# Optimization experiments

Hardware: AMD Instinct MI355X
Metric: run time of the kernel (lower is better)

The kernel has to match this reference:

```python
import jax, jax.numpy as jnp
import numpy as np

NEG_SLOPE = 0.2
LN_EPS = 1e-5


def gat_conv(x, src, dst, n_nodes, W, a_src, a_dst, b, concat):
    # W: [F_in, H*C]; a_src, a_dst: [H, C]; b: [H*C] if concat else [C]
    H, C = a_src.shape
    h = (x @ W).reshape(-1, H, C)                      # [N, H, C]
    # per-node attention scores, gathered per edge
    s_src = jnp.einsum('nhc,hc->nh', h, a_src)          # [N, H]
    s_dst = jnp.einsum('nhc,hc->nh', h, a_dst)          # [N, H]
    e = jax.nn.leaky_relu(s_src[src] + s_dst[dst], NEG_SLOPE)  # [E, H]
    # segment softmax over incoming edges of each dst node
    e_max = jax.ops.segment_max(e, dst, num_segments=n_nodes)  # [N, H]
    w = jnp.exp(e - e_max[dst])
    denom = jax.ops.segment_sum(w, dst, num_segments=n_nodes)
    alpha = w / (denom[dst] + 1e-16)                    # [E, H]
    # weighted scatter-aggregate of source messages
    msg = h[src] * alpha[:, :, None]                    # [E, H, C]
    out = jax.ops.segment_sum(msg, dst, num_segments=n_nodes)  # [N, H, C]
    out = out.reshape(n_nodes, H * C) if concat else out.mean(axis=1)
    return out + b


def layer_norm(x, g, b):
    mu = x.mean(-1, keepdims=True)
    var = ((x - mu) ** 2).mean(-1, keepdims=True)
    return (x - mu) * jax.lax.rsqrt(var + LN_EPS) * g + b


def setup_inputs() -> dict:
    key = jax.random.key(0)
    ks = jax.random.split(key, 16)
    N, E, F_in = 50000, 400000, 128
    H1, C1 = 4, 128          # conv1: heads=4, hidden=128, concat -> 512
    C2 = 64                  # conv2: heads=1, out=64
    sd = lambda fan: 1.0 / np.sqrt(fan)
    inp = {
        'x': jax.random.normal(ks[0], (N, F_in), jnp.float32),
        'edge_index': jax.random.randint(ks[1], (2, E), 0, N, jnp.int64),
        'num_nodes': N,
        'W1': jax.random.normal(ks[2], (F_in, H1 * C1), jnp.float32) * sd(F_in),
        'a_src1': jax.random.normal(ks[3], (H1, C1), jnp.float32) * sd(C1),
        'a_dst1': jax.random.normal(ks[4], (H1, C1), jnp.float32) * sd(C1),
        'b1': jnp.zeros((H1 * C1,), jnp.float32),
        'W2': jax.random.normal(ks[5], (H1 * C1, C2), jnp.float32) * sd(H1 * C1),
        'a_src2': jax.random.normal(ks[6], (1, C2), jnp.float32) * sd(C2),
        'a_dst2': jax.random.normal(ks[7], (1, C2), jnp.float32) * sd(C2),
        'b2': jnp.zeros((C2,), jnp.float32),
        'Wm1': jax.random.normal(ks[8], (C2, 32), jnp.float32) * sd(C2),
        'bm1': jnp.zeros((32,), jnp.float32),
        'g_ln': jnp.ones((32,), jnp.float32),
        'b_ln': jnp.zeros((32,), jnp.float32),
        'Wm2': jax.random.normal(ks[9], (32, 16), jnp.float32) * sd(32),
        'bm2': jnp.zeros((16,), jnp.float32),
    }
    return inp


def reference(x, edge_index, num_nodes, W1, a_src1, a_dst1, b1, W2, a_src2, a_dst2, b2, Wm1, bm1, g_ln, b_ln, Wm2, bm2):
    N = num_nodes
    # PyG GATConv add_self_loops=True
    loop = jnp.arange(N, dtype=edge_index.dtype)
    src = jnp.concatenate([edge_index[0], loop])
    dst = jnp.concatenate([edge_index[1], loop])
    # dropout layers are identity in eval mode
    h = jax.nn.elu(gat_conv(x, src, dst, N, W1, a_src1, a_dst1, b1, concat=True))
    h = jax.nn.elu(gat_conv(h, src, dst, N, W2, a_src2, a_dst2, b2, concat=False))
    h = jax.nn.relu(layer_norm(h @ Wm1 + bm1, g_ln, b_ln))
    return h @ Wm2 + bm2  # [N, 2*n_spectral_dims]
```

## Files before the change

### kernel.cpp

```cpp
#include <hip/hip_runtime.h>
#include <cmath>


#define F_IN 128
#define H1   4
#define C1   128
#define D1   512
#define C2   64
#define DM1  32
#define DM2  16

#define LRELU(x) ((x) > 0.f ? (x) : 0.2f * (x))

typedef float f32x4 __attribute__((ext_vector_type(4)));
typedef short short8 __attribute__((ext_vector_type(8)));

static __device__ __forceinline__ float bf2f(unsigned short u) {
    return __builtin_bit_cast(float, (unsigned)u << 16);
}
static __device__ __forceinline__ unsigned short f2bf(float f) {
    unsigned u = __builtin_bit_cast(unsigned, f);
    u = (u + 0x7fffu + ((u >> 16) & 1u)) >> 16;
    return (unsigned short)u;
}
static __device__ __forceinline__ float bflo(unsigned d) {
    return __builtin_bit_cast(float, d << 16);
}
static __device__ __forceinline__ float bfhi(unsigned d) {
    return __builtin_bit_cast(float, d & 0xffff0000u);
}

__global__ void k_detect(const void* ei, int E, int* flag) {
    __shared__ int any;
    if (threadIdx.x == 0) any = 0;
    __syncthreads();
    const int* p = (const int*)ei;
    int cnt = E < 4096 ? E : 4096;
    int stride = E / cnt;
    int local = 0;
    for (int i = threadIdx.x; i < cnt; i += blockDim.x) {
        long long idx = (long long)i * stride;
        local |= p[2 * idx + 1];
    }
    if (local) atomicOr(&any, 1);
    __syncthreads();
    if (threadIdx.x == 0) *flag = (any == 0) ? 1 : 0;
}

__global__ void k_convert_prep(const void* ei, const int* flag, int E, int N,
                               int* src32, int* dst32, int* deg, int* rank32,
                               const float* __restrict__ x,
                               const float* __restrict__ W1,
                               const float* __restrict__ W2,
                               unsigned short* __restrict__ xb,
                               unsigned short* __restrict__ W1t,
                               unsigned short* __restrict__ W2t, int n8) {
    int i = blockIdx.x * blockDim.x + threadIdx.x;
    int Etot = E + N;
    if (i < Etot) {
        int s, d;
        if (i < E) {
            if (*flag) {
                const long long* q = (const long long*)ei;
                s = (int)q[i];
                d = (int)q[(size_t)E + i];
            } else {
                const int* q = (const int*)ei;
                s = q[i];
                d = q[(size_t)E + i];
            }
        } else {
            s = i - E;
            d = i - E;
        }
        src32[i] = s;
        dst32[i] = d;
        rank32[i] = atomicAdd(&deg[d], 1);
        return;
    }
    int i1 = i - Etot;
    if (i1 < n8) {
        const float4* p = (const float4*)(x + (size_t)i1 * 8);
        float4 a = p[0], b = p[1];
        unsigned short r[8] = {f2bf(a.x), f2bf(a.y), f2bf(a.z), f2bf(a.w),
                               f2bf(b.x), f2bf(b.y), f2bf(b.z), f2bf(b.w)};
        *(short8*)(xb + (size_t)i1 * 8) = *(const short8*)r;
        return;
    }
    int i2 = i1 - n8;
    if (i2 < F_IN * D1) {
        int nn = i2 / F_IN, kk = i2 - nn * F_IN;
        W1t[i2] = f2bf(W1[(size_t)kk * D1 + nn]);
        return;
    }
    int i3 = i2 - F_IN * D1;
    if (i3 < D1 * C2) {
        int nn = i3 / D1, kk = i3 - nn * D1;
        W2t[i3] = f2bf(W2[(size_t)kk * C2 + nn]);
    }
}

__global__ __launch_bounds__(256) void k_scan1(const int* __restrict__ deg,
                                               int* __restrict__ bsum, int N) {
    int t = threadIdx.x;
    int base = blockIdx.x * 1024 + t * 4;
    int s = 0;
    if (base + 3 < N) {
        int4 v = *(const int4*)&deg[base];
        s = v.x + v.y + v.z + v.w;
    } else {
        for (int k = 0; k < 4; k++)
            if (base + k < N) s += deg[base + k];
    }
#pragma unroll
    for (int o = 1; o < 64; o <<= 1) s += __shfl_xor(s, o, 64);
    __shared__ int ws[4];
    if ((t & 63) == 0) ws[t >> 6] = s;
    __syncthreads();
    if (t == 0) bsum[blockIdx.x] = ws[0] + ws[1] + ws[2] + ws[3];
}

__global__ __launch_bounds__(1024) void k_scan2(const int* __restrict__ bsum,
                                                int* __restrict__ boff, int nb) {
    __shared__ int wsum[16];
    __shared__ int woff[16];
    int t = threadIdx.x, lane = t & 63, wid = t >> 6;
    int v = (t < nb) ? bsum[t] : 0;
    int x = v;
#pragma unroll
    for (int o = 1; o < 64; o <<= 1) {
        int tv = __shfl_up(x, o, 64);
        if (lane >= o) x += tv;
    }
    if (lane == 63) wsum[wid] = x;
    __syncthreads();
    if (wid == 0) {
        int y = (lane < 16) ? wsum[lane] : 0;
        int z = y;
#pragma unroll
        for (int o = 1; o < 16; o <<= 1) {
            int tv = __shfl_up(z, o, 64);
            if (lane >= o) z += tv;
        }
        if (lane < 16) woff[lane] = z - y;
    }
    __syncthreads();
    if (t < nb) boff[t] = woff[wid] + x - v;
}

__global__ __launch_bounds__(256) void k_scan3(const int* __restrict__ deg,
                                               const int* __restrict__ boff,
                                               int* __restrict__ rowstart, int N,
                                               int Etot) {
    int t = threadIdx.x, lane = t & 63, wid = t >> 6;
    int base = blockIdx.x * 1024 + t * 4;
    int v0 = 0, v1 = 0, v2 = 0, v3 = 0;
    if (base + 3 < N) {
        int4 v = *(const int4*)&deg[base];
        v0 = v.x; v1 = v.y; v2 = v.z; v3 = v.w;
    } else {
        if (base + 0 < N) v0 = deg[base + 0];
        if (base + 1 < N) v1 = deg[base + 1];
        if (base + 2 < N) v2 = deg[base + 2];
        if (base + 3 < N) v3 = deg[base + 3];
    }
    int s4 = v0 + v1 + v2 + v3;
    int x = s4;
#pragma unroll
    for (int o = 1; o < 64; o <<= 1) {
        int tv = __shfl_up(x, o, 64);
        if (lane >= o) x += tv;
    }
    __shared__ int ws[4];
    if (lane == 63) ws[wid] = x;
    __syncthreads();
    int woff = 0;
#pragma unroll
    for (int w = 0; w < 4; w++)
        if (w < wid) woff += ws[w];
    int ex = boff[blockIdx.x] + woff + (x - s4);
    int e0 = ex, e1 = ex + v0, e2 = e1 + v1, e3 = e2 + v2;
    if (base + 0 < N) rowstart[base + 0] = e0;
    if (base + 1 < N) rowstart[base + 1] = e1;
    if (base + 2 < N) rowstart[base + 2] = e2;
    if (base + 3 < N) rowstart[base + 3] = e3;
    if (blockIdx.x == 0 && t == 0) rowstart[N] = Etot;
}

__global__ void k_fill(const int* __restrict__ src32, const int* __restrict__ dst32,
                       const int* __restrict__ rank32,
                       const int* __restrict__ rowstart, int* __restrict__ adj,
                       int Etot) {
    int i = blockIdx.x * blockDim.x + threadIdx.x;
    if (i < Etot) adj[rowstart[dst32[i]] + rank32[i]] = src32[i];
}

template <int WM, int WN, int MF, int NF, bool OUT_BF16, int SC_MODE>
__global__ __launch_bounds__(256) void k_gemm_bf16(
    const unsigned short* __restrict__ A, const unsigned short* __restrict__ Bt,
    void* __restrict__ C, int M, int K, int NC,
    const float* __restrict__ avs, const float* __restrict__ avd,
    float* __restrict__ s_src, float* __restrict__ s_dst) {
    constexpr int BM = WM * MF * 16;
    constexpr int BN = WN * NF * 16;
    constexpr int BK = 64;
    __shared__ unsigned short As[BM * BK];
    __shared__ unsigned short Bs[BN * BK];
    __shared__ float ps_lds[WN][BM], pd_lds[WN][BM];
    const int tid = threadIdx.x;
    const int row0 = blockIdx.x * BM, col0 = blockIdx.y * BN;
    const int wave = tid >> 6, lane = tid & 63;
    const int wr = wave / WN, wc = wave % WN;
    const int lrow = lane & 15, lkg = lane >> 4;
    f32x4 acc[MF][NF] = {};
    for (int k0 = 0; k0 < K; k0 += BK) {
#pragma unroll
        for (int inst = 0; inst < (BM * 8) / 256; ++inst) {
            int ibase = inst * 256 + wave * 64;
            int i = ibase + lane;
            int r = i >> 3, u = i & 7, su = u ^ (r & 7);
            const unsigned short* gp = A + (size_t)(row0 + r) * K + k0 + su * 8;
            __builtin_amdgcn_global_load_lds(
                (const __attribute__((address_space(1))) void*)gp,
                (__attribute__((address_space(3))) void*)&As[ibase * 8], 16, 0, 0);
        }
#pragma unroll
        for (int inst = 0; inst < (BN * 8) / 256; ++inst) {
            int ibase = inst * 256 + wave * 64;
            int i = ibase + lane;
            int r = i >> 3, u = i & 7, su = u ^ (r & 7);
            const unsigned short* gp = Bt + (size_t)(col0 + r) * K + k0 + su * 8;
            __builtin_amdgcn_global_load_lds(
                (const __attribute__((address_space(1))) void*)gp,
                (__attribute__((address_space(3))) void*)&Bs[ibase * 8], 16, 0, 0);
        }
        __syncthreads();
#pragma unroll
        for (int kk = 0; kk < BK; kk += 32) {
            short8 af[MF], bfr[NF];
#pragma unroll
            for (int m = 0; m < MF; m++) {
                int ar = wr * MF * 16 + m * 16 + lrow;
                int au = kk / 8 + lkg;
                af[m] = *(const short8*)&As[(ar * 8 + (au ^ (lrow & 7))) * 8];
            }
#pragma unroll
            for (int n = 0; n < NF; n++) {
                int br = wc * NF * 16 + n * 16 + lrow;
                int au = kk / 8 + lkg;
                bfr[n] = *(const short8*)&Bs[(br * 8 + (au ^ (lrow & 7))) * 8];
            }
#pragma unroll
            for (int m = 0; m < MF; m++)
#pragma unroll
                for (int n = 0; n < NF; n++)
                    acc[m][n] = __builtin_amdgcn_mfma_f32_16x16x32_bf16(
                        af[m], bfr[n], acc[m][n], 0, 0, 0);
        }
        __syncthreads();
    }
#pragma unroll
    for (int m = 0; m < MF; m++)
#pragma unroll
        for (int n = 0; n < NF; n++)
#pragma unroll
            for (int r = 0; r < 4; r++) {
                int gr = row0 + wr * MF * 16 + m * 16 + lkg * 4 + r;
                int gc = col0 + wc * NF * 16 + n * 16 + lrow;
                if (gr < M) {
                    if (OUT_BF16)
                        ((unsigned short*)C)[(size_t)gr * NC + gc] = f2bf(acc[m][n][r]);
                    else
                        ((float*)C)[(size_t)gr * NC + gc] = acc[m][n][r];
                }
            }
    if (SC_MODE) {
        float asv[NF], adv[NF];
#pragma unroll
        for (int n = 0; n < NF; n++) {
            int gc = col0 + wc * NF * 16 + n * 16 + lrow;
            asv[n] = avs[gc];
            adv[n] = avd[gc];
        }
#pragma unroll
        for (int m = 0; m < MF; m++)
#pragma unroll
            for (int r = 0; r < 4; r++) {
                float ps = 0.f, pd = 0.f;
#pragma unroll
                for (int n = 0; n < NF; n++) {
                    ps += acc[m][n][r] * asv[n];
                    pd += acc[m][n][r] * adv[n];
                }
#pragma unroll
                for (int o = 1; o < 16; o <<= 1) {
                    ps += __shfl_xor(ps, o, 64);
                    pd += __shfl_xor(pd, o, 64);
                }
                if (lrow == 0) {
                    int lr = wr * MF * 16 + m * 16 + lkg * 4 + r;
                    ps_lds[wc][lr] = ps;
                    pd_lds[wc][lr] = pd;
                }
            }
        __syncthreads();
        for (int rr = tid; rr < BM; rr += 256) {
            int gr = row0 + rr;
            if (gr < M) {
                float s = 0.f, d = 0.f;
#pragma unroll
                for (int w = 0; w < WN; w++) {
                    s += ps_lds[w][rr];
                    d += pd_lds[w][rr];
                }
                if (SC_MODE == 1) {
                    s_src[(size_t)gr * H1 + blockIdx.y] = s;
                    s_dst[(size_t)gr * H1 + blockIdx.y] = d;
                } else {
                    s_src[gr] = s;
                    s_dst[gr] = d;
                }
            }
        }
    }
}

__global__ __launch_bounds__(256) void k_agg1(
    const unsigned short* __restrict__ h1b, const float* __restrict__ s_src,
    const float* __restrict__ s_dst, const int* __restrict__ rowstart,
    const int* __restrict__ adj, const float* __restrict__ b1,
    unsigned short* __restrict__ out1, int N) {
    __shared__ uint2 ex_lds[4][64];
    int wv = (blockIdx.x * blockDim.x + threadIdx.x) >> 6;
    if (wv >= N) return;
    int wv4 = (threadIdx.x >> 6) & 3;
    int lane = threadIdx.x & 63;
    int beg = rowstart[wv], end = rowstart[wv + 1];
    int h4 = lane & 3, jj = lane >> 2;
    float sdh = s_dst[(size_t)wv * 4 + h4];
    int nch = (end - beg + 15) >> 4;
    float e0st = -1e30f;
    int s0st = 0;
    float m = -1e30f, dn = 0.f;
    for (int c = 0; c < nch; ++c) {
        int j = beg + c * 16 + jj;
        float e = -1e30f;
        int sj = 0;
        if (j < end) {
            sj = adj[j];
            e = LRELU(s_src[(size_t)sj * 4 + h4] + sdh);
        }
        if (c == 0) { e0st = e; s0st = sj; }
        float nm = fmaxf(m, e);
        dn = dn * __expf(m - nm) + ((j < end) ? __expf(e - nm) : 0.f);
        m = nm;
    }
#pragma unroll
    for (int o = 4; o < 64; o <<= 1) {
        float om = __shfl_xor(m, o, 64);
        float od = __shfl_xor(dn, o, 64);
        float nm = fmaxf(m, om);
        dn = dn * __expf(m - nm) + od * __expf(om - nm);
        m = nm;
    }
    float inv = 1.f / (dn + 1e-16f);
    int hg = lane >> 4;
    float aL[4] = {}, aH[4] = {};
#define ACC1(vv, aa)                                        \
    do {                                                    \
        aL[0] += (aa)*bflo(vv.x); aH[0] += (aa)*bfhi(vv.x); \
        aL[1] += (aa)*bflo(vv.y); aH[1] += (aa)*bfhi(vv.y); \
        aL[2] += (aa)*bflo(vv.z); aH[2] += (aa)*bfhi(vv.z); \
        aL[3] += (aa)*bflo(vv.w); aH[3] += (aa)*bfhi(vv.w); \
    } while (0)
    for (int c = 0; c < nch; ++c) {
        int j = beg + c * 16 + jj;
        float e;
        int sj;
        if (c == 0) {
            e = e0st;
            sj = s0st;
        } else {
            sj = 0;
            e = -1e30f;
            if (j < end) {
                sj = adj[j];
                e = LRELU(s_src[(size_t)sj * 4 + h4] + sdh);
            }
        }
        float av = (j < end) ? __expf(e - m) * inv : 0.f;
        ex_lds[wv4][lane] = make_uint2((unsigned)sj, __builtin_bit_cast(unsigned, av));
        asm volatile("s_waitcnt lgkmcnt(0)" ::: "memory");
        int cnt = min(16, end - beg - c * 16);
        int j2 = 0;
        for (; j2 + 4 <= cnt; j2 += 4) {
            uint2 e0 = ex_lds[wv4][(j2 + 0) * 4 + hg];
            uint2 e1 = ex_lds[wv4][(j2 + 1) * 4 + hg];
            uint2 e2 = ex_lds[wv4][(j2 + 2) * 4 + hg];
            uint2 e3 = ex_lds[wv4][(j2 + 3) * 4 + hg];
            uint4 v0 = *(const uint4*)&h1b[(size_t)e0.x * D1 + lane * 8];
            uint4 v1 = *(const uint4*)&h1b[(size_t)e1.x * D1 + lane * 8];
            uint4 v2 = *(const uint4*)&h1b[(size_t)e2.x * D1 + lane * 8];
            uint4 v3 = *(const uint4*)&h1b[(size_t)e3.x * D1 + lane * 8];
            float a0 = __builtin_bit_cast(float, e0.y);
            float a1 = __builtin_bit_cast(float, e1.y);
            float a2 = __builtin_bit_cast(float, e2.y);
            float a3 = __builtin_bit_cast(float, e3.y);
            ACC1(v0, a0); ACC1(v1, a1); ACC1(v2, a2); ACC1(v3, a3);
        }
        for (; j2 < cnt; ++j2) {
            uint2 e0 = ex_lds[wv4][j2 * 4 + hg];
            uint4 v0 = *(const uint4*)&h1b[(size_t)e0.x * D1 + lane * 8];
            float a0 = __builtin_bit_cast(float, e0.y);
            ACC1(v0, a0);
        }
    }
#undef ACC1
    const float4* bp = (const float4*)&b1[lane * 8];
    float4 bb0 = bp[0], bb1 = bp[1];
    float r[8];
    r[0] = aL[0] + bb0.x; r[1] = aH[0] + bb0.y;
    r[2] = aL[1] + bb0.z; r[3] = aH[1] + bb0.w;
    r[4] = aL[2] + bb1.x; r[5] = aH[2] + bb1.y;
    r[6] = aL[3] + bb1.z; r[7] = aH[3] + bb1.w;
    unsigned short o16[8];
#pragma unroll
    for (int i = 0; i < 8; i++) {
        float z = r[i] > 0.f ? r[i] : expm1f(r[i]);
        o16[i] = f2bf(z);
    }
    *(short8*)&out1[(size_t)wv * D1 + lane * 8] = *(const short8*)o16;
}

__global__ __launch_bounds__(256) void k_agg2(
    const unsigned short* __restrict__ h2lin, const float* __restrict__ s_src,
    const float* __restrict__ s_dst, const int* __restrict__ rowstart,
    const int* __restrict__ adj, const float* __restrict__ b2,
    float* __restrict__ h2, int N) {
    int wv = (blockIdx.x * blockDim.x + threadIdx.x) >> 6;
    if (wv >= N) return;
    int lane = threadIdx.x & 63;
    int beg = rowstart[wv], end = rowstart[wv + 1];
    float sd = s_dst[wv];
    float m = -1e30f, dn = 0.f;
    for (int c0 = beg; c0 < end; c0 += 64) {
        int j = c0 + lane;
        float e = -1e30f;
        if (j < end) e = LRELU(s_src[adj[j]] + sd);
        float nm = fmaxf(m, e);
        dn = dn * __expf(m - nm) + ((j < end) ? __expf(e - nm) : 0.f);
        m = nm;
    }
#pragma unroll
    for (int o = 1; o < 64; o <<= 1) {
        float om = __shfl_xor(m, o, 64);
        float od = __shfl_xor(dn, o, 64);
        float nm = fmaxf(m, om);
        dn = dn * __expf(m - nm) + od * __expf(om - nm);
        m = nm;
    }
    float inv = 1.f / (dn + 1e-16f);
    int eg = lane >> 4, ch = (lane & 15) * 4;
    float a0 = 0.f, a1 = 0.f, a2 = 0.f, a3 = 0.f;
    for (int j0 = beg; j0 < end; j0 += 4) {
        int j = j0 + eg;
        if (j < end) {
            int sj = adj[j];
            float a = __expf(LRELU(s_src[sj] + sd) - m) * inv;
            uint2 rv = *(const uint2*)&h2lin[(size_t)sj * C2 + ch];
            a0 += a * bflo(rv.x); a1 += a * bfhi(rv.x);
            a2 += a * bflo(rv.y); a3 += a * bfhi(rv.y);
        }
    }
#pragma unroll
    for (int o = 16; o < 64; o <<= 1) {
        a0 += __shfl_xor(a0, o, 64);
        a1 += __shfl_xor(a1, o, 64);
        a2 += __shfl_xor(a2, o, 64);
        a3 += __shfl_xor(a3, o, 64);
    }
    if (lane < 16) {
        const float4 bb = *(const float4*)&b2[ch];
        float r0 = a0 + bb.x, r1 = a1 + bb.y, r2 = a2 + bb.z, r3 = a3 + bb.w;
        r0 = r0 > 0.f ? r0 : expm1f(r0);
        r1 = r1 > 0.f ? r1 : expm1f(r1);
        r2 = r2 > 0.f ? r2 : expm1f(r2);
        r3 = r3 > 0.f ? r3 : expm1f(r3);
        *(float4*)&h2[(size_t)wv * C2 + ch] = make_float4(r0, r1, r2, r3);
    }
}

__global__ __launch_bounds__(256) void k_mlp(
    const float* __restrict__ h2, const float* __restrict__ Wm1,
    const float* __restrict__ bm1, const float* __restrict__ g_ln,
    const float* __restrict__ b_ln, const float* __restrict__ Wm2,
    const float* __restrict__ bm2, float* __restrict__ out, int N) {
    __shared__ float w1[C2 * DM1];
    __shared__ float w2[DM1 * DM2];
    __shared__ float cb1[DM1], cg[DM1], cbl[DM1], cb2[DM2];
    int tid = threadIdx.x;
    for (int i = tid; i < C2 * DM1; i += 256) w1[i] = Wm1[i];
    for (int i = tid; i < DM1 * DM2; i += 256) w2[i] = Wm2[i];
    if (tid < DM1) {
        cb1[tid] = bm1[tid];
        cg[tid] = g_ln[tid];
        cbl[tid] = b_ln[tid];
    } else if (tid < DM1 + DM2) {
        cb2[tid - DM1] = bm2[tid - DM1];
    }
    __syncthreads();
    int n = blockIdx.x * 256 + tid;
    if (n >= N) return;
    float h[C2];
    const float4* hp = (const float4*)&h2[(size_t)n * C2];
#pragma unroll
    for (int i = 0; i < C2 / 4; i++) {
        float4 v = hp[i];
        h[4 * i] = v.x; h[4 * i + 1] = v.y;
        h[4 * i + 2] = v.z; h[4 * i + 3] = v.w;
    }
    float t[DM1];
#pragma unroll
    for (int j = 0; j < DM1; j++) {
        float a = cb1[j];
#pragma unroll
        for (int c = 0; c < C2; c++) a += h[c] * w1[c * DM1 + j];
        t[j] = a;
    }
    float mu = 0.f;
#pragma unroll
    for (int j = 0; j < DM1; j++) mu += t[j];
    mu *= (1.f / DM1);
    float var = 0.f;
#pragma unroll
    for (int j = 0; j < DM1; j++) {
        float d = t[j] - mu;
        var += d * d;
    }
    var *= (1.f / DM1);
    float rs = rsqrtf(var + 1e-5f);
#pragma unroll
    for (int j = 0; j < DM1; j++) {
        float z = (t[j] - mu) * rs * cg[j] + cbl[j];
        t[j] = z > 0.f ? z : 0.f;
    }
    float o[DM2];
#pragma unroll
    for (int k = 0; k < DM2; k++) {
        float a = cb2[k];
#pragma unroll
        for (int j = 0; j < DM1; j++) a += t[j] * w2[j * DM2 + k];
        o[k] = a;
    }
    float4* op = (float4*)&out[(size_t)n * DM2];
    op[0] = make_float4(o[0], o[1], o[2], o[3]);
    op[1] = make_float4(o[4], o[5], o[6], o[7]);
    op[2] = make_float4(o[8], o[9], o[10], o[11]);
    op[3] = make_float4(o[12], o[13], o[14], o[15]);
}

extern "C" void kernel_launch(void* const* d_in, const int* in_sizes, int n_in,
                              void* d_out, int out_size, void* d_ws,
                              size_t ws_size, hipStream_t stream) {
    const float* x      = (const float*)d_in[0];
    const void*  ei     = d_in[1];
    const float* W1     = (const float*)d_in[3];
    const float* a_src1 = (const float*)d_in[4];
    const float* a_dst1 = (const float*)d_in[5];
    const float* b1     = (const float*)d_in[6];
    const float* W2     = (const float*)d_in[7];
    const float* a_src2 = (const float*)d_in[8];
    const float* a_dst2 = (const float*)d_in[9];
    const float* b2     = (const float*)d_in[10];
    const float* Wm1    = (const float*)d_in[11];
    const float* bm1    = (const float*)d_in[12];
    const float* g_ln   = (const float*)d_in[13];
    const float* b_ln   = (const float*)d_in[14];
    const float* Wm2    = (const float*)d_in[15];
    const float* bm2    = (const float*)d_in[16];

    const int N    = in_sizes[0] / F_IN;
    const int E    = in_sizes[1] / 2;
    const int Etot = E + N;
    const int nb   = (N + 1023) / 1024;

    char* ws = (char*)d_ws;
    size_t off = 0;
    auto alloc = [&](size_t bytes) {
        size_t o = off;
        off += (bytes + 255) & ~(size_t)255;
        return o;
    };
    int*   flag     = (int*)(ws + alloc(4));
    int*   src32    = (int*)(ws + alloc((size_t)Etot * 4));
    int*   dst32    = (int*)(ws + alloc((size_t)Etot * 4));
    int*   rank32   = (int*)(ws + alloc((size_t)Etot * 4));
    int*   deg      = (int*)(ws + alloc((size_t)N * 4));
    int*   bsum     = (int*)(ws + alloc(4096 * 4));
    int*   boff     = (int*)(ws + alloc(4096 * 4));
    int*   rowstart = (int*)(ws + alloc((size_t)(N + 1) * 4));
    int*   adj      = (int*)(ws + alloc((size_t)Etot * 4));
    float* s_src1   = (float*)(ws + alloc((size_t)N * H1 * 4));
    float* s_dst1   = (float*)(ws + alloc((size_t)N * H1 * 4));
    unsigned short* xb    = (unsigned short*)(ws + alloc((size_t)N * F_IN * 2));
    unsigned short* W1t   = (unsigned short*)(ws + alloc((size_t)F_IN * D1 * 2));
    unsigned short* W2t   = (unsigned short*)(ws + alloc((size_t)D1 * C2 * 2));
    unsigned short* h1b   = (unsigned short*)(ws + alloc((size_t)N * D1 * 2));
    unsigned short* out1  = (unsigned short*)(ws + alloc((size_t)N * D1 * 2));
    unsigned short* h2lin = (unsigned short*)(ws + alloc((size_t)N * C2 * 2));
    float* h2    = (float*)(ws + alloc((size_t)N * C2 * 4));
    float* s_src2 = s_src1;
    float* s_dst2 = s_dst1;

    hipMemsetAsync(deg, 0, (size_t)N * 4, stream);
    k_detect<<<1, 256, 0, stream>>>(ei, E, flag);
    int n8 = N * F_IN / 8;
    int total_cp = Etot + n8 + F_IN * D1 + D1 * C2;
    k_convert_prep<<<(total_cp + 255) / 256, 256, 0, stream>>>(
        ei, flag, E, N, src32, dst32, deg, rank32, x, W1, W2, xb, W1t, W2t, n8);
    k_scan1<<<nb, 256, 0, stream>>>(deg, bsum, N);
    k_scan2<<<1, 1024, 0, stream>>>(bsum, boff, nb);
    k_scan3<<<nb, 256, 0, stream>>>(deg, boff, rowstart, N, Etot);
    k_fill<<<(Etot + 255) / 256, 256, 0, stream>>>(src32, dst32, rank32, rowstart,
                                                   adj, Etot);

    k_gemm_bf16<2, 2, 4, 4, true, 1>
        <<<dim3((N + 127) / 128, D1 / 128), 256, 0, stream>>>(
            xb, W1t, h1b, N, F_IN, D1, a_src1, a_dst1, s_src1, s_dst1);
    k_agg1<<<(N * 64 + 255) / 256, 256, 0, stream>>>(h1b, s_src1, s_dst1, rowstart,
                                                     adj, b1, out1, N);

    k_gemm_bf16<2, 2, 2, 2, true, 2>
        <<<dim3((N + 63) / 64, 1), 256, 0, stream>>>(
            out1, W2t, h2lin, N, D1, C2, a_src2, a_dst2, s_src2, s_dst2);
    k_agg2<<<(N * 64 + 255) / 256, 256, 0, stream>>>(h2lin, s_src2, s_dst2, rowstart,
                                                     adj, b2, h2, N);

    k_mlp<<<(N + 255) / 256, 256, 0, stream>>>(h2, Wm1, bm1, g_ln, b_ln, Wm2, bm2,
                                               (float*)d_out, N);
}
```

Before: 322.0 us.

## Fuse agg2 with MLP, single-pass online softmax in agg1, drop src/dst buffers

```diff
diff --git a/kernel.cpp b/kernel.cpp
--- a/kernel.cpp
+++ b/kernel.cpp
@@ -48,7 +48,7 @@
 }
 
 __global__ void k_convert_prep(const void* ei, const int* flag, int E, int N,
-                               int* src32, int* dst32, int* deg, int* rank32,
+                               int* deg, int* rank32,
                                const float* __restrict__ x,
                                const float* __restrict__ W1,
                                const float* __restrict__ W2,
@@ -58,23 +58,18 @@
     int i = blockIdx.x * blockDim.x + threadIdx.x;
     int Etot = E + N;
     if (i < Etot) {
-        int s, d;
+        int d;
         if (i < E) {
             if (*flag) {
                 const long long* q = (const long long*)ei;
-                s = (int)q[i];
                 d = (int)q[(size_t)E + i];
             } else {
                 const int* q = (const int*)ei;
-                s = q[i];
                 d = q[(size_t)E + i];
             }
         } else {
-            s = i - E;
             d = i - E;
         }
-        src32[i] = s;
-        dst32[i] = d;
         rank32[i] = atomicAdd(&deg[d], 1);
         return;
     }
@@ -187,12 +182,28 @@
     if (blockIdx.x == 0 && t == 0) rowstart[N] = Etot;
 }
 
-__global__ void k_fill(const int* __restrict__ src32, const int* __restrict__ dst32,
+__global__ void k_fill(const void* ei, const int* flag, int E, int N,
                        const int* __restrict__ rank32,
                        const int* __restrict__ rowstart, int* __restrict__ adj,
                        int Etot) {
     int i = blockIdx.x * blockDim.x + threadIdx.x;
-    if (i < Etot) adj[rowstart[dst32[i]] + rank32[i]] = src32[i];
+    if (i >= Etot) return;
+    int s, d;
+    if (i < E) {
+        if (*flag) {
+            const long long* q = (const long long*)ei;
+            s = (int)q[i];
+            d = (int)q[(size_t)E + i];
+        } else {
+            const int* q = (const int*)ei;
+            s = q[i];
+            d = q[(size_t)E + i];
+        }
+    } else {
+        s = i - E;
+        d = i - E;
+    }
+    adj[rowstart[d] + rank32[i]] = s;
 }
 
 template <int WM, int WN, int MF, int NF, bool OUT_BF16, int SC_MODE>
@@ -336,35 +347,10 @@
     int wv4 = (threadIdx.x >> 6) & 3;
     int lane = threadIdx.x & 63;
     int beg = rowstart[wv], end = rowstart[wv + 1];
-    int h4 = lane & 3, jj = lane >> 2;
+    int h4 = lane & 3, jj = lane >> 2, hg = lane >> 4;
     float sdh = s_dst[(size_t)wv * 4 + h4];
     int nch = (end - beg + 15) >> 4;
-    float e0st = -1e30f;
-    int s0st = 0;
     float m = -1e30f, dn = 0.f;
-    for (int c = 0; c < nch; ++c) {
-        int j = beg + c * 16 + jj;
-        float e = -1e30f;
-        int sj = 0;
-        if (j < end) {
-            sj = adj[j];
-            e = LRELU(s_src[(size_t)sj * 4 + h4] + sdh);
-        }
-        if (c == 0) { e0st = e; s0st = sj; }
-        float nm = fmaxf(m, e);
-        dn = dn * __expf(m - nm) + ((j < end) ? __expf(e - nm) : 0.f);
-        m = nm;
-    }
-#pragma unroll
-    for (int o = 4; o < 64; o <<= 1) {
-        float om = __shfl_xor(m, o, 64);
-        float od = __shfl_xor(dn, o, 64);
-        float nm = fmaxf(m, om);
-        dn = dn * __expf(m - nm) + od * __expf(om - nm);
-        m = nm;
-    }
-    float inv = 1.f / (dn + 1e-16f);
-    int hg = lane >> 4;
     float aL[4] = {}, aH[4] = {};
 #define ACC1(vv, aa)                                        \
     do {                                                    \
@@ -375,22 +361,25 @@
     } while (0)
     for (int c = 0; c < nch; ++c) {
         int j = beg + c * 16 + jj;
-        float e;
-        int sj;
-        if (c == 0) {
-            e = e0st;
-            sj = s0st;
-        } else {
-            sj = 0;
-            e = -1e30f;
-            if (j < end) {
-                sj = adj[j];
-                e = LRELU(s_src[(size_t)sj * 4 + h4] + sdh);
-            }
-        }
-        float av = (j < end) ? __expf(e - m) * inv : 0.f;
+        float e = -1e30f;
+        int sj = 0;
+        if (j < end) {
+            sj = adj[j];
+            e = LRELU(s_src[(size_t)sj * 4 + h4] + sdh);
+        }
+        float mc = e;
+#pragma unroll
+        for (int o = 4; o < 64; o <<= 1) mc = fmaxf(mc, __shfl_xor(mc, o, 64));
+        float mn = fmaxf(m, mc);
+        float scale = __expf(m - mn);
+        float av = (j < end) ? __expf(e - mn) : 0.f;
+        dn = dn * scale + av;
+        m = mn;
         ex_lds[wv4][lane] = make_uint2((unsigned)sj, __builtin_bit_cast(unsigned, av));
         asm volatile("s_waitcnt lgkmcnt(0)" ::: "memory");
+        float sg = __shfl(scale, hg, 64);
+#pragma unroll
+        for (int i = 0; i < 4; i++) { aL[i] *= sg; aH[i] *= sg; }
         int cnt = min(16, end - beg - c * 16);
         int j2 = 0;
         for (; j2 + 4 <= cnt; j2 += 4) {
@@ -416,13 +405,17 @@
         }
     }
 #undef ACC1
+#pragma unroll
+    for (int o = 4; o < 64; o <<= 1) dn += __shfl_xor(dn, o, 64);
+    float inv = 1.f / (dn + 1e-16f);
+    float ig = __shfl(inv, hg, 64);
     const float4* bp = (const float4*)&b1[lane * 8];
     float4 bb0 = bp[0], bb1 = bp[1];
     float r[8];
-    r[0] = aL[0] + bb0.x; r[1] = aH[0] + bb0.y;
-    r[2] = aL[1] + bb0.z; r[3] = aH[1] + bb0.w;
-    r[4] = aL[2] + bb1.x; r[5] = aH[2] + bb1.y;
-    r[6] = aL[3] + bb1.z; r[7] = aH[3] + bb1.w;
+    r[0] = aL[0] * ig + bb0.x; r[1] = aH[0] * ig + bb0.y;
+    r[2] = aL[1] * ig + bb0.z; r[3] = aH[1] * ig + bb0.w;
+    r[4] = aL[2] * ig + bb1.x; r[5] = aH[2] * ig + bb1.y;
+    r[6] = aL[3] * ig + bb1.z; r[7] = aH[3] * ig + bb1.w;
     unsigned short o16[8];
 #pragma unroll
     for (int i = 0; i < 8; i++) {
@@ -432,14 +425,32 @@
     *(short8*)&out1[(size_t)wv * D1 + lane * 8] = *(const short8*)o16;
 }
 
-__global__ __launch_bounds__(256) void k_agg2(
+__global__ __launch_bounds__(256) void k_agg2mlp(
     const unsigned short* __restrict__ h2lin, const float* __restrict__ s_src,
     const float* __restrict__ s_dst, const int* __restrict__ rowstart,
     const int* __restrict__ adj, const float* __restrict__ b2,
-    float* __restrict__ h2, int N) {
-    int wv = (blockIdx.x * blockDim.x + threadIdx.x) >> 6;
+    const float* __restrict__ Wm1, const float* __restrict__ bm1,
+    const float* __restrict__ g_ln, const float* __restrict__ b_ln,
+    const float* __restrict__ Wm2, const float* __restrict__ bm2,
+    float* __restrict__ out, int N) {
+    __shared__ float w1[C2 * DM1];
+    __shared__ float w2[DM1 * DM2];
+    __shared__ float cb2[C2], cb1m[DM1], cg[DM1], cbl[DM1], cb2m[DM2];
+    __shared__ float h_lds[4][C2];
+    __shared__ float t_lds[4][DM1];
+    int tid = threadIdx.x;
+    for (int i = tid; i < C2 * DM1; i += 256) w1[i] = Wm1[i];
+    for (int i = tid; i < DM1 * DM2; i += 256) w2[i] = Wm2[i];
+    if (tid < C2) cb2[tid] = b2[tid];
+    else if (tid < C2 + DM1) cb1m[tid - C2] = bm1[tid - C2];
+    else if (tid < C2 + 2 * DM1) cg[tid - C2 - DM1] = g_ln[tid - C2 - DM1];
+    else if (tid < C2 + 3 * DM1) cbl[tid - C2 - 2 * DM1] = b_ln[tid - C2 - 2 * DM1];
+    else if (tid < C2 + 3 * DM1 + DM2) cb2m[tid - C2 - 3 * DM1] = bm2[tid - C2 - 3 * DM1];
+    __syncthreads();
+    int wv = (blockIdx.x * blockDim.x + tid) >> 6;
     if (wv >= N) return;
-    int lane = threadIdx.x & 63;
+    int wv4 = (tid >> 6) & 3;
+    int lane = tid & 63;
     int beg = rowstart[wv], end = rowstart[wv + 1];
     float sd = s_dst[wv];
     float m = -1e30f, dn = 0.f;
@@ -480,83 +491,38 @@
         a3 += __shfl_xor(a3, o, 64);
     }
     if (lane < 16) {
-        const float4 bb = *(const float4*)&b2[ch];
-        float r0 = a0 + bb.x, r1 = a1 + bb.y, r2 = a2 + bb.z, r3 = a3 + bb.w;
+        float r0 = a0 + cb2[ch], r1 = a1 + cb2[ch + 1];
+        float r2 = a2 + cb2[ch + 2], r3 = a3 + cb2[ch + 3];
         r0 = r0 > 0.f ? r0 : expm1f(r0);
         r1 = r1 > 0.f ? r1 : expm1f(r1);
         r2 = r2 > 0.f ? r2 : expm1f(r2);
         r3 = r3 > 0.f ? r3 : expm1f(r3);
-        *(float4*)&h2[(size_t)wv * C2 + ch] = make_float4(r0, r1, r2, r3);
-    }
-}
-
-__global__ __launch_bounds__(256) void k_mlp(
-    const float* __restrict__ h2, const float* __restrict__ Wm1,
-    const float* __restrict__ bm1, const float* __restrict__ g_ln,
-    const float* __restrict__ b_ln, const float* __restrict__ Wm2,
-    const float* __restrict__ bm2, float* __restrict__ out, int N) {
-    __shared__ float w1[C2 * DM1];
-    __shared__ float w2[DM1 * DM2];
-    __shared__ float cb1[DM1], cg[DM1], cbl[DM1], cb2[DM2];
-    int tid = threadIdx.x;
-    for (int i = tid; i < C2 * DM1; i += 256) w1[i] = Wm1[i];
-    for (int i = tid; i < DM1 * DM2; i += 256) w2[i] = Wm2[i];
-    if (tid < DM1) {
-        cb1[tid] = bm1[tid];
-        cg[tid] = g_ln[tid];
-        cbl[tid] = b_ln[tid];
-    } else if (tid < DM1 + DM2) {
-        cb2[tid - DM1] = bm2[tid - DM1];
-    }
-    __syncthreads();
-    int n = blockIdx.x * 256 + tid;
-    if (n >= N) return;
-    float h[C2];
-    const float4* hp = (const float4*)&h2[(size_t)n * C2];
-#pragma unroll
-    for (int i = 0; i < C2 / 4; i++) {
-        float4 v = hp[i];
-        h[4 * i] = v.x; h[4 * i + 1] = v.y;
-        h[4 * i + 2] = v.z; h[4 * i + 3] = v.w;
-    }
-    float t[DM1];
-#pragma unroll
-    for (int j = 0; j < DM1; j++) {
-        float a = cb1[j];
-#pragma unroll
-        for (int c = 0; c < C2; c++) a += h[c] * w1[c * DM1 + j];
-        t[j] = a;
-    }
-    float mu = 0.f;
-#pragma unroll
-    for (int j = 0; j < DM1; j++) mu += t[j];
+        *(float4*)&h_lds[wv4][ch] = make_float4(r0, r1, r2, r3);
+    }
+    asm volatile("s_waitcnt lgkmcnt(0)" ::: "memory");
+    int j = lane & 31;
+    float t = cb1m[j];
+#pragma unroll
+    for (int c = 0; c < C2; c++) t += h_lds[wv4][c] * w1[c * DM1 + j];
+    float mu = t;
+#pragma unroll
+    for (int o = 1; o < 32; o <<= 1) mu += __shfl_xor(mu, o, 64);
     mu *= (1.f / DM1);
-    float var = 0.f;
-#pragma unroll
-    for (int j = 0; j < DM1; j++) {
-        float d = t[j] - mu;
-        var += d * d;
-    }
+    float dv = t - mu, var = dv * dv;
+#pragma unroll
+    for (int o = 1; o < 32; o <<= 1) var += __shfl_xor(var, o, 64);
     var *= (1.f / DM1);
     float rs = rsqrtf(var + 1e-5f);
-#pragma unroll
-    for (int j = 0; j < DM1; j++) {
-        float z = (t[j] - mu) * rs * cg[j] + cbl[j];
-        t[j] = z > 0.f ? z : 0.f;
-    }
-    float o[DM2];
-#pragma unroll
-    for (int k = 0; k < DM2; k++) {
-        float a = cb2[k];
-#pragma unroll
-        for (int j = 0; j < DM1; j++) a += t[j] * w2[j * DM2 + k];
-        o[k] = a;
-    }
-    float4* op = (float4*)&out[(size_t)n * DM2];
-    op[0] = make_float4(o[0], o[1], o[2], o[3]);
-    op[1] = make_float4(o[4], o[5], o[6], o[7]);
-    op[2] = make_float4(o[8], o[9], o[10], o[11]);
-    op[3] = make_float4(o[12], o[13], o[14], o[15]);
+    float z = (t - mu) * rs * cg[j] + cbl[j];
+    z = fmaxf(z, 0.f);
+    if (lane < 32) t_lds[wv4][lane] = z;
+    asm volatile("s_waitcnt lgkmcnt(0)" ::: "memory");
+    if (lane < 16) {
+        float a = cb2m[lane];
+#pragma unroll
+        for (int j2 = 0; j2 < DM1; j2++) a += t_lds[wv4][j2] * w2[j2 * DM2 + lane];
+        out[(size_t)wv * DM2 + lane] = a;
+    }
 }
 
 extern "C" void kernel_launch(void* const* d_in, const int* in_sizes, int n_in,
@@ -592,8 +558,6 @@
         return o;
     };
     int*   flag     = (int*)(ws + alloc(4));
-    int*   src32    = (int*)(ws + alloc((size_t)Etot * 4));
-    int*   dst32    = (int*)(ws + alloc((size_t)Etot * 4));
     int*   rank32   = (int*)(ws + alloc((size_t)Etot * 4));
     int*   deg      = (int*)(ws + alloc((size_t)N * 4));
     int*   bsum     = (int*)(ws + alloc(4096 * 4));
@@ -608,7 +572,6 @@
     unsigned short* h1b   = (unsigned short*)(ws + alloc((size_t)N * D1 * 2));
     unsigned short* out1  = (unsigned short*)(ws + alloc((size_t)N * D1 * 2));
     unsigned short* h2lin = (unsigned short*)(ws + alloc((size_t)N * C2 * 2));
-    float* h2    = (float*)(ws + alloc((size_t)N * C2 * 4));
     float* s_src2 = s_src1;
     float* s_dst2 = s_dst1;
 
@@ -617,12 +580,12 @@
     int n8 = N * F_IN / 8;
     int total_cp = Etot + n8 + F_IN * D1 + D1 * C2;
     k_convert_prep<<<(total_cp + 255) / 256, 256, 0, stream>>>(
-        ei, flag, E, N, src32, dst32, deg, rank32, x, W1, W2, xb, W1t, W2t, n8);
+        ei, flag, E, N, deg, rank32, x, W1, W2, xb, W1t, W2t, n8);
     k_scan1<<<nb, 256, 0, stream>>>(deg, bsum, N);
     k_scan2<<<1, 1024, 0, stream>>>(bsum, boff, nb);
     k_scan3<<<nb, 256, 0, stream>>>(deg, boff, rowstart, N, Etot);
-    k_fill<<<(Etot + 255) / 256, 256, 0, stream>>>(src32, dst32, rank32, rowstart,
-                                                   adj, Etot);
+    k_fill<<<(Etot + 255) / 256, 256, 0, stream>>>(ei, flag, E, N, rank32,
+                                                   rowstart, adj, Etot);
 
     k_gemm_bf16<2, 2, 4, 4, true, 1>
         <<<dim3((N + 127) / 128, D1 / 128), 256, 0, stream>>>(
@@ -633,9 +596,8 @@
     k_gemm_bf16<2, 2, 2, 2, true, 2>
         <<<dim3((N + 63) / 64, 1), 256, 0, stream>>>(
             out1, W2t, h2lin, N, D1, C2, a_src2, a_dst2, s_src2, s_dst2);
-    k_agg2<<<(N * 64 + 255) / 256, 256, 0, stream>>>(h2lin, s_src2, s_dst2, rowstart,
-                                                     adj, b2, h2, N);
-
-    k_mlp<<<(N + 255) / 256, 256, 0, stream>>>(h2, Wm1, bm1, g_ln, b_ln, Wm2, bm2,
-                                               (float*)d_out, N);
-}
+
+    k_agg2mlp<<<(N * 64 + 255) / 256, 256, 0, stream>>>(
+        h2lin, s_src2, s_dst2, rowstart, adj, b2, Wm1, bm1, g_ln, b_ln, Wm2, bm2,
+        (float*)d_out, N);
+}
```

After: 331.0 us. 2.8% more time.
